# Kernel tuning notes

Measured on AMD Instinct MI355X. Metric: run time of the kernel, lower is better.

Reference implementation:

```python
import jax, jax.numpy as jnp
import numpy as np

B, T, F = 256, 2048, 20
H_NODES = 256


def _heaviside(x):
    # smooth heaviside approx used throughout the original module
    return (jnp.tanh(10.0 * x) + 1.0) * 0.5


def _evap(wu, wl, wd, pet):
    h = _heaviside
    et1 = h(wu - pet) * pet + h(pet - wu) * wu
    rp = h(pet - et1) * (pet - et1)  # h(-(pet-et1))*0 term vanishes
    et22 = h(rp - wl) * wl + h(wl - rp) * rp
    et2 = h(rp) * et22
    et33 = h(rp - et2 - wd) * wd + h(wd - (rp - et2)) * (rp - et2)
    et3 = h(rp - et2) * et33
    return et1, et2, et3


def _runoff(wu, wl, wd, p, wum, wlm, wdm, b, c):
    wum = wum * 19.9 + 0.1
    wlm = wlm * 30.0 + 60.0
    wdm = wdm * 60.0 + 60.0
    c = c * 0.19 + 0.01
    b = b * 0.3 + 0.1
    w_total = wum + wlm + wdm
    s = c * (wu / w_total) ** 2 + b * (wl / w_total) ** 2
    return _heaviside(p - s) * (p - s)


def _partition(runoff, k1, k2, k3):
    k1 = k1 * 0.69 + 0.01
    k2 = k2 * 0.69 + 0.01
    k3 = k3 * 0.89 + 0.01
    sr = k1 * runoff
    itf = k2 * (runoff - sr)
    bf = k3 * (runoff - sr - itf)
    return sr, itf, bf


def setup_inputs() -> dict:
    key = jax.random.key(0)
    ks = jax.random.split(key, 7)
    u = lambda k, shp: jax.random.uniform(k, shp, jnp.float32, -0.05, 0.05)
    inputs = jax.random.uniform(ks[0], (B, T, F), jnp.float32)
    return {
        "inputs": inputs,
        "w1": u(ks[1], (15, H_NODES)),
        "b1": jnp.zeros((H_NODES,), jnp.float32),
        "w2": u(ks[2], (H_NODES, 64)),
        "b2": jnp.zeros((64,), jnp.float32),
        "w3": u(ks[3], (64, 8)),
        "b3": jnp.zeros((8,), jnp.float32),
    }


def reference(inputs, w1, b1, w2, b2, w3, b3):
    pet = inputs[..., 0:1]
    tmean = inputs[..., 1:2]
    p = inputs[..., 2:3]
    attrs = inputs[..., 5:]  # [B,T,15]

    # static-attribute -> physical-parameter MLP
    h1 = jnp.tanh(attrs @ w1 + b1)
    h2 = jnp.tanh(h1 @ w2 + b2)
    params = jax.nn.sigmoid(h2 @ w3 + b3)  # [B,T,8]

    xs = jnp.concatenate([pet, p, tmean, params], axis=-1)  # [B,T,11]

    def step(state, x):
        wu, wl, wd = state[:, 0:1], state[:, 1:2], state[:, 2:3]
        pet_t, p_t = x[:, 0:1], x[:, 1:2]
        et1, et2, et3 = _evap(wu, wl, wd, pet_t)
        clip = lambda d: jnp.clip(d, -1e5, 1e5)
        wu_n = wu + clip(p_t - et1)
        wl_n = wl + clip(p_t - et1 - et2)
        wd_n = wd + clip(p_t - et1 - et2 - et3)
        ns = jnp.concatenate([wu_n, wl_n, wd_n], axis=1)  # [B,3]
        return ns, ns

    init = jnp.zeros((inputs.shape[0], 3), inputs.dtype)
    _, outs = jax.lax.scan(step, init, jnp.swapaxes(xs, 0, 1))  # [T,B,3]
    outputs = jnp.swapaxes(outs, 0, 1)  # [B,T,3]

    wu, wl, wd = outputs[..., 0:1], outputs[..., 1:2], outputs[..., 2:3]
    wum, wlm, wdm = params[..., 0:1], params[..., 1:2], params[..., 2:3]
    b, c = params[..., 3:4], params[..., 4:5]
    k1, k2, k3 = params[..., 5:6], params[..., 6:7], params[..., 7:8]

    et1, et2, et3 = _evap(wu, wl, wd, pet)
    # NOTE: original call() swaps (wl,wd) and (wlm,wdm) here - kept faithful
    runoff = _runoff(wu, wd, wl, p, wum, wdm, wlm, b, c)
    sr, itf, bf = _partition(runoff, k1, k2, k3)
    total_q = sr + itf * 0.5 + bf * 0.25  # flow routing
    return total_q  # [B,T,1]
```

## Files before the change

### kernel.cpp

```cpp
#include <hip/hip_runtime.h>

#define B_ 256
#define T_ 2048
#define F_ 20
#define NT (B_*T_)
#define CH 16
#define NCH (T_/CH)

typedef __bf16 bf16x8 __attribute__((ext_vector_type(8)));
typedef float  f32x4  __attribute__((ext_vector_type(4)));

__device__ __forceinline__ float ex2(float x){ return __builtin_amdgcn_exp2f(x); }
__device__ __forceinline__ float rcpf_(float x){ return __builtin_amdgcn_rcpf(x); }

#define K10F 28.853900817779268f
#define K1F   2.8853900817779268f
#define LOG2E 1.4426950408889634f

__device__ __forceinline__ float hside(float x){ return 1.0f - rcpf_(ex2(K10F*x) + 1.0f); }
__device__ __forceinline__ float tanh_f(float z){ return 1.0f - 2.0f*rcpf_(ex2(K1F*z) + 1.0f); }
__device__ __forceinline__ float sigmoid_f(float z){ return rcpf_(1.0f + ex2(-LOG2E*z)); }


__global__ __launch_bounds__(256) void prep_kernel(const float* __restrict__ in,
                                                   float* __restrict__ ws){
  int r = blockIdx.x*256 + threadIdx.x;
  if (r >= NT) return;
  int b = r & (B_-1);
  int t = r >> 8;
  const float* src = in + ((size_t)b*T_ + t)*F_;
  ((float2*)ws)[r] = make_float2(src[0], src[2]);
}

__global__ __launch_bounds__(512) void fused_kernel(const float* __restrict__ in,
    const float* __restrict__ w1, const float* __restrict__ b1,
    const float* __restrict__ w2, const float* __restrict__ b2,
    const float* __restrict__ w3, const float* __restrict__ b3,
    float* __restrict__ ws){
  extern __shared__ char sm[];
  float* pk4 = ws + 4*(size_t)NT;

  if (blockIdx.x < 4) {
    asm volatile("s_setprio 3");
    const float2* pp2 = (const float2*)ws;
    float* wuT = ws + 2*(size_t)NT;
    float* wdT = ws + 3*(size_t)NT;
    float*  d1L = (float*)sm;
    float*  bsQ = (float*)(sm + 8192);
    float2* rhL = (float2*)(sm + 24576);
    float2* qbL = (float2*)(sm + 40960);

    int tid = threadIdx.x;
    int wv = tid >> 6, lane = tid & 63;
    int boff = blockIdx.x * 64;

    float wu = 0.0f, wl = 0.0f, wd = 0.0f;
    float2 buf[2][8];

    if (wv == 0){
      #pragma unroll
      for (int g = 0; g < 2; ++g)
        #pragma unroll
        for (int i = 0; i < 8; ++i)
          buf[g][i] = pp2[(g*8 + i)*B_ + boff + lane];
    }

    for (int it = 0; it < NCH + 3; ++it){
      if (wv == 0){
        if (it < NCH){
          int c = it, par = c & 1;
          #pragma unroll
          for (int g = 0; g < 2; ++g){
            #pragma unroll
            for (int i = 0; i < 8; ++i){
              int s = g*8 + i;
              float pet = buf[g][i].x, p = buf[g][i].y;
              float d  = wu - pet;
              float r1 = rcpf_(ex2(K10F*d) + 1.0f);
              float d1 = -d*r1;
              float base = (p - pet) + d1;
              wu += base;
              wuT[(c*CH + s)*B_ + boff + lane] = wu;
              d1L[par*(CH*64) + s*64 + lane] = d1;
              bsQ[(c&3)*(CH*64) + s*64 + lane] = base;
            }
            int cn = (c + 1 < NCH) ? c + 1 : c;
            #pragma unroll
            for (int i = 0; i < 8; ++i)
              buf[g][i] = pp2[(cn*CH + g*8 + i)*B_ + boff + lane];
          }
        }
      } else if (wv == 1){
        if (it >= 1 && it <= NCH){
          int c = it - 1, par = c & 1;
          #pragma unroll
          for (int s = 0; s < CH; ++s){
            float d1 = d1L[par*(CH*64) + s*64 + lane];
            float r2 = rcpf_(ex2(K10F*d1) + 1.0f);
            float rp = fmaf(-d1, r2, d1);
            float hrp = 1.0f - rcpf_(ex2(K10F*rp) + 1.0f);
            rhL[par*(CH*64) + s*64 + lane] = make_float2(rp, hrp);
          }
        }
      } else if (wv == 2){
        if (it >= 2 && it <= NCH + 1){
          int c = it - 2, par = c & 1;
          #pragma unroll
          for (int s = 0; s < CH; ++s){
            float2 rh  = rhL[par*(CH*64) + s*64 + lane];
            float base = bsQ[(c&3)*(CH*64) + s*64 + lane];
            float d2   = rh.x - wl;
            float r    = rcpf_(ex2(K10F*d2) + 1.0f);
            float et22 = fmaf(d2, r, wl);
            float et2  = rh.y * et22;
            float b2   = base - et2;
            wl += b2;
            qbL[par*(CH*64) + s*64 + lane] = make_float2(rh.x - et2, b2);
          }
        }
      } else if (wv == 3){
        if (it >= 3){
          int c = it - 3, par = c & 1;
          #pragma unroll
          for (int s = 0; s < CH; ++s){
            float2 qb  = qbL[par*(CH*64) + s*64 + lane];
            float hqv  = 1.0f - rcpf_(ex2(K10F*qb.x) + 1.0f);
            float d3   = qb.x - wd;
            float r    = rcpf_(ex2(K10F*d3) + 1.0f);
            float et33 = fmaf(d3, r, wd);
            float et3  = hqv * et33;
            wd += qb.y - et3;
            wdT[(c*CH + s)*B_ + boff + lane] = wd;
          }
        }
      }
      __syncthreads();
    }
    return;
  }

  __bf16* w1f  = (__bf16*)sm;
  __bf16* w2f  = (__bf16*)(sm + 8192);
  float*  b1s  = (float*)(sm + 40960);
  float*  b2s  = (float*)(sm + 41984);
  float*  w3s  = (float*)(sm + 42240);
  float*  b3s  = (float*)(sm + 44288);
  __bf16* hbufA= (__bf16*)(sm + 44320);

  int tid = threadIdx.x;

  for (int s = tid; s < 16*32*8; s += 512) w1f[s] = (__bf16)0.0f;
  __syncthreads();
  for (int idx = tid; idx < 15*256; idx += 512){
    int k = idx >> 8, n = idx & 255;
    int ct = n >> 4;
    int l  = ((k>>3)*16) + (n & 15);
    int j  = k & 7;
    w1f[(ct*32 + l)*8 + j] = (__bf16)w1[idx];
  }
  for (int idx = tid; idx < 256*64; idx += 512){
    int k = idx >> 6, n = idx & 63;
    int kb = k >> 5;
    int lq = (k >> 3) & 3;
    int j  = k & 7;
    int ct = n >> 4;
    int l  = lq*16 + (n & 15);
    w2f[((kb*4 + ct)*64 + l)*8 + j] = (__bf16)w2[idx];
  }
  if (tid < 256) b1s[tid] = b1[tid];
  if (tid < 64)  b2s[tid] = b2[tid];
  if (tid < 512) w3s[tid] = w3[tid];
  if (tid < 8)   b3s[tid] = b3[tid];
  __syncthreads();

  int lane = tid & 63;
  int wv   = tid >> 6;
  int m    = lane & 15;
  int q    = lane >> 4;
  int r0   = (blockIdx.x - 4)*128 + wv*16;

  int rowA = r0 + m;
  int bA = rowA & (B_-1), tA = rowA >> 8;
  const float* ap = in + ((size_t)bA*T_ + tA)*F_ + 5;
  bf16x8 a1;
  #pragma unroll
  for (int j = 0; j < 8; ++j){
    int k = q*8 + j;
    float v = (k < 15) ? ap[k] : 0.0f;
    a1[j] = (__bf16)v;
  }

  __bf16* hb = hbufA + wv*1152;
  f32x4 zero4 = {0.0f, 0.0f, 0.0f, 0.0f};
  bf16x8 zero8;
  #pragma unroll
  for (int j = 0; j < 8; ++j) zero8[j] = (__bf16)0.0f;

  f32x4 acc2[4] = {zero4, zero4, zero4, zero4};

  #pragma unroll
  for (int p = 0; p < 4; ++p){
    #pragma unroll
    for (int c4 = 0; c4 < 4; ++c4){
      int ct = p*4 + c4;
      bf16x8 bw = zero8;
      if (lane < 32) bw = *(const bf16x8*)&w1f[(ct*32 + lane)*8];
      f32x4 c1 = __builtin_amdgcn_mfma_f32_16x16x32_bf16(a1, bw, zero4, 0, 0, 0);
      int f = c4*16 + m;
      float bb = b1s[p*64 + f];
      #pragma unroll
      for (int i = 0; i < 4; ++i){
        float h = tanh_f(c1[i] + bb);
        hb[(q*4 + i)*72 + f] = (__bf16)h;
      }
    }
    #pragma unroll
    for (int kb = 0; kb < 2; ++kb){
      bf16x8 a2 = *(const bf16x8*)&hb[m*72 + q*8 + kb*32];
      #pragma unroll
      for (int ct = 0; ct < 4; ++ct){
        bf16x8 bw2 = *(const bf16x8*)&w2f[(((p*2 + kb)*4 + ct)*64 + lane)*8];
        acc2[ct] = __builtin_amdgcn_mfma_f32_16x16x32_bf16(a2, bw2, acc2[ct], 0, 0, 0);
      }
    }
  }

  #pragma unroll
  for (int ct = 0; ct < 4; ++ct){
    int f = ct*16 + m;
    float bb = b2s[f];
    #pragma unroll
    for (int i = 0; i < 4; ++i){
      float h = tanh_f(acc2[ct][i] + bb);
      hb[(q*4 + i)*72 + f] = (__bf16)h;
    }
  }

  float z0 = b3s[2*q], z1 = b3s[2*q + 1];
  #pragma unroll
  for (int kb3 = 0; kb3 < 8; ++kb3){
    bf16x8 hv8 = *(const bf16x8*)&hb[m*72 + kb3*8];
    #pragma unroll
    for (int j = 0; j < 8; ++j){
      float hv = (float)hv8[j];
      int k = kb3*8 + j;
      z0 = fmaf(hv, w3s[k*8 + 2*q],     z0);
      z1 = fmaf(hv, w3s[k*8 + 2*q + 1], z1);
    }
  }

  float* hf = (float*)hb;
  hf[m*8 + 2*q]     = sigmoid_f(z0);
  hf[m*8 + 2*q + 1] = sigmoid_f(z1);
  if (q == 0){
    float P0=hf[m*8+0], P1=hf[m*8+1], P2=hf[m*8+2], P3=hf[m*8+3];
    float P4=hf[m*8+4], P5=hf[m*8+5], P6=hf[m*8+6], P7=hf[m*8+7];
    float wum = fmaf(P0, 19.9f, 0.1f);
    float wlm = fmaf(P2, 30.0f, 60.0f);
    float wdm = fmaf(P1, 60.0f, 60.0f);
    float wt  = wum + wlm + wdm;
    float rw  = 1.0f / wt;
    float cc  = fmaf(P4, 0.19f, 0.01f);
    float bc  = fmaf(P3, 0.30f, 0.10f);
    float A   = cc*rw*rw;
    float Bc  = bc*rw*rw;
    float k1  = fmaf(P5, 0.69f, 0.01f);
    float k2  = fmaf(P6, 0.69f, 0.01f);
    float k3  = fmaf(P7, 0.89f, 0.01f);
    float KP  = k1 + 0.5f*k2*(1.0f-k1) + 0.25f*k3*(1.0f-k1)*(1.0f-k2);
    int rowO = r0 + m;
    *(float4*)&pk4[(size_t)rowO*4] = make_float4(A, Bc, KP, 0.0f);
  }
}

__global__ __launch_bounds__(256) void final_kernel(const float* __restrict__ ws,
                                                    float* __restrict__ out){
  __shared__ float tile[64*65];
  int tb = blockIdx.x & 31;
  int bb = blockIdx.x >> 5;
  int t0 = tb*64, b0 = bb*64;
  int tid = threadIdx.x;
  const float2* pp2 = (const float2*)ws;
  const float* wuT  = ws + 2*(size_t)NT;
  const float* wdT  = ws + 3*(size_t)NT;
  const float* pk4  = ws + 4*(size_t)NT;

  #pragma unroll
  for (int k = 0; k < 16; ++k){
    int idx = k*256 + tid;
    int tl = idx >> 6, bl = idx & 63;
    int r = (t0 + tl)*B_ + b0 + bl;
    float p  = pp2[r].y;
    float wu = wuT[r], wd = wdT[r];
    float4 k4 = *(const float4*)&pk4[(size_t)r*4];
    float ps = p - k4.x*wu*wu - k4.y*wd*wd;
    float runoff = hside(ps)*ps;
    tile[bl*65 + tl] = k4.z * runoff;
  }
  __syncthreads();
  #pragma unroll
  for (int k = 0; k < 16; ++k){
    int idx = k*256 + tid;
    int tl2 = idx & 63, bl2 = idx >> 6;
    out[(size_t)(b0 + bl2)*T_ + t0 + tl2] = tile[bl2*65 + tl2];
  }
}

extern "C" void kernel_launch(void* const* d_in, const int* in_sizes, int n_in,
                              void* d_out, int out_size, void* d_ws, size_t ws_size,
                              hipStream_t stream) {
  const float* in = (const float*)d_in[0];
  const float* w1 = (const float*)d_in[1];
  const float* b1 = (const float*)d_in[2];
  const float* w2 = (const float*)d_in[3];
  const float* b2 = (const float*)d_in[4];
  const float* w3 = (const float*)d_in[5];
  const float* b3 = (const float*)d_in[6];
  float* out = (float*)d_out;
  float* ws  = (float*)d_ws;

  prep_kernel <<<NT/256,     256, 0,     stream>>>(in, ws);
  fused_kernel<<<NT/128 + 4, 512, 62752, stream>>>(in, w1, b1, w2, b2, w3, b3, ws);
  final_kernel<<<128,        256, 0,     stream>>>(ws, out);
}
```

Measured before the change: 215.4 us.

## Double rows per MLP block, stage w2 in halves, run layer3 on MFMA

Each wave of the MLP blocks now handles 32 rows instead of 16, which halves the block count and amortises per-block weight staging over twice the work. w2 is loaded into shared memory in two halves with extra barriers, so the shared footprint stays small. Layer 3 moves from scalar FMAs to MFMA, using a hi/lo bf16 split of w3 to keep precision close to the fp32 version. The costs are more registers per thread and extra synchronisation, and this may interact with the co-scheduled scan blocks that share the same grid.

```diff
diff --git a/kernel.cpp b/kernel.cpp
--- a/kernel.cpp
+++ b/kernel.cpp
@@ -113,9 +113,9 @@
             float r    = rcpf_(ex2(K10F*d2) + 1.0f);
             float et22 = fmaf(d2, r, wl);
             float et2  = rh.y * et22;
-            float b2   = base - et2;
-            wl += b2;
-            qbL[par*(CH*64) + s*64 + lane] = make_float2(rh.x - et2, b2);
+            float b2v  = base - et2;
+            wl += b2v;
+            qbL[par*(CH*64) + s*64 + lane] = make_float2(rh.x - et2, b2v);
           }
         }
       } else if (wv == 3){
@@ -139,17 +139,45 @@
     return;
   }
 
-  __bf16* w1f  = (__bf16*)sm;
-  __bf16* w2f  = (__bf16*)(sm + 8192);
-  float*  b1s  = (float*)(sm + 40960);
-  float*  b2s  = (float*)(sm + 41984);
-  float*  w3s  = (float*)(sm + 42240);
-  float*  b3s  = (float*)(sm + 44288);
-  __bf16* hbufA= (__bf16*)(sm + 44320);
-
-  int tid = threadIdx.x;
-
-  for (int s = tid; s < 16*32*8; s += 512) w1f[s] = (__bf16)0.0f;
+  __bf16* w1f   = (__bf16*)sm;
+  __bf16* w2f   = (__bf16*)(sm + 8192);
+  float*  b1s   = (float*)(sm + 24576);
+  float*  b2s   = (float*)(sm + 25600);
+  float*  b3s   = (float*)(sm + 25856);
+  __bf16* hbufA = (__bf16*)(sm + 25888);
+
+  int tid  = threadIdx.x;
+  int lane = tid & 63;
+  int wv   = tid >> 6;
+  int m    = lane & 15;
+  int q    = lane >> 4;
+  int r0   = (blockIdx.x - 4)*256 + wv*32;
+
+  bf16x8 a1[2];
+  #pragma unroll
+  for (int u = 0; u < 2; ++u){
+    int rowA = r0 + u*16 + m;
+    int bA = rowA & (B_-1), tA = rowA >> 8;
+    const float* ap = in + ((size_t)bA*T_ + tA)*F_ + 5;
+    #pragma unroll
+    for (int j = 0; j < 8; ++j){
+      int k = q*8 + j;
+      a1[u][j] = (__bf16)((k < 15) ? ap[k] : 0.0f);
+    }
+  }
+  bf16x8 w3h[2], w3l[2];
+  #pragma unroll
+  for (int kb = 0; kb < 2; ++kb){
+    #pragma unroll
+    for (int j = 0; j < 8; ++j){
+      float v = (m < 8) ? w3[(kb*32 + q*8 + j)*8 + m] : 0.0f;
+      __bf16 hi = (__bf16)v;
+      w3h[kb][j] = hi;
+      w3l[kb][j] = (__bf16)(v - (float)hi);
+    }
+  }
+
+  ((float4*)sm)[tid] = make_float4(0.0f, 0.0f, 0.0f, 0.0f);
   __syncthreads();
   for (int idx = tid; idx < 15*256; idx += 512){
     int k = idx >> 8, n = idx & 255;
@@ -158,69 +186,74 @@
     int j  = k & 7;
     w1f[(ct*32 + l)*8 + j] = (__bf16)w1[idx];
   }
-  for (int idx = tid; idx < 256*64; idx += 512){
-    int k = idx >> 6, n = idx & 63;
-    int kb = k >> 5;
-    int lq = (k >> 3) & 3;
-    int j  = k & 7;
-    int ct = n >> 4;
-    int l  = lq*16 + (n & 15);
-    w2f[((kb*4 + ct)*64 + l)*8 + j] = (__bf16)w2[idx];
+  for (int idx = tid; idx < 8192; idx += 512){
+    int kk = idx >> 6, n = idx & 63;
+    int kb2 = kk >> 5;
+    int lq  = (kk >> 3) & 3;
+    int j   = kk & 7;
+    int ct  = n >> 4;
+    int l   = lq*16 + (n & 15);
+    w2f[((kb2*4 + ct)*64 + l)*8 + j] = (__bf16)w2[kk*64 + n];
   }
   if (tid < 256) b1s[tid] = b1[tid];
   if (tid < 64)  b2s[tid] = b2[tid];
-  if (tid < 512) w3s[tid] = w3[tid];
   if (tid < 8)   b3s[tid] = b3[tid];
   __syncthreads();
 
-  int lane = tid & 63;
-  int wv   = tid >> 6;
-  int m    = lane & 15;
-  int q    = lane >> 4;
-  int r0   = (blockIdx.x - 4)*128 + wv*16;
-
-  int rowA = r0 + m;
-  int bA = rowA & (B_-1), tA = rowA >> 8;
-  const float* ap = in + ((size_t)bA*T_ + tA)*F_ + 5;
-  bf16x8 a1;
-  #pragma unroll
-  for (int j = 0; j < 8; ++j){
-    int k = q*8 + j;
-    float v = (k < 15) ? ap[k] : 0.0f;
-    a1[j] = (__bf16)v;
-  }
-
-  __bf16* hb = hbufA + wv*1152;
   f32x4 zero4 = {0.0f, 0.0f, 0.0f, 0.0f};
   bf16x8 zero8;
   #pragma unroll
   for (int j = 0; j < 8; ++j) zero8[j] = (__bf16)0.0f;
 
-  f32x4 acc2[4] = {zero4, zero4, zero4, zero4};
-
-  #pragma unroll
-  for (int p = 0; p < 4; ++p){
-    #pragma unroll
-    for (int c4 = 0; c4 < 4; ++c4){
-      int ct = p*4 + c4;
-      bf16x8 bw = zero8;
-      if (lane < 32) bw = *(const bf16x8*)&w1f[(ct*32 + lane)*8];
-      f32x4 c1 = __builtin_amdgcn_mfma_f32_16x16x32_bf16(a1, bw, zero4, 0, 0, 0);
-      int f = c4*16 + m;
-      float bb = b1s[p*64 + f];
-      #pragma unroll
-      for (int i = 0; i < 4; ++i){
-        float h = tanh_f(c1[i] + bb);
-        hb[(q*4 + i)*72 + f] = (__bf16)h;
-      }
-    }
-    #pragma unroll
-    for (int kb = 0; kb < 2; ++kb){
-      bf16x8 a2 = *(const bf16x8*)&hb[m*72 + q*8 + kb*32];
-      #pragma unroll
-      for (int ct = 0; ct < 4; ++ct){
-        bf16x8 bw2 = *(const bf16x8*)&w2f[(((p*2 + kb)*4 + ct)*64 + lane)*8];
-        acc2[ct] = __builtin_amdgcn_mfma_f32_16x16x32_bf16(a2, bw2, acc2[ct], 0, 0, 0);
+  __bf16* hb = hbufA + wv*2304;
+  f32x4 acc2[2][4] = {{zero4, zero4, zero4, zero4},
+                      {zero4, zero4, zero4, zero4}};
+
+  #pragma unroll
+  for (int pc = 0; pc < 2; ++pc){
+    if (pc == 1){
+      __syncthreads();
+      for (int idx = tid; idx < 8192; idx += 512){
+        int kk = idx >> 6, n = idx & 63;
+        int kb2 = kk >> 5;
+        int lq  = (kk >> 3) & 3;
+        int j   = kk & 7;
+        int ct  = n >> 4;
+        int l   = lq*16 + (n & 15);
+        w2f[((kb2*4 + ct)*64 + l)*8 + j] = (__bf16)w2[(128 + kk)*64 + n];
+      }
+      __syncthreads();
+    }
+    #pragma unroll
+    for (int ph = 0; ph < 2; ++ph){
+      int p = pc*2 + ph;
+      #pragma unroll
+      for (int c4 = 0; c4 < 4; ++c4){
+        int ct = p*4 + c4;
+        bf16x8 bw = zero8;
+        if (lane < 32) bw = *(const bf16x8*)&w1f[(ct*32 + lane)*8];
+        int f = c4*16 + m;
+        float bb = b1s[p*64 + f];
+        #pragma unroll
+        for (int u = 0; u < 2; ++u){
+          f32x4 c1 = __builtin_amdgcn_mfma_f32_16x16x32_bf16(a1[u], bw, zero4, 0, 0, 0);
+          #pragma unroll
+          for (int i = 0; i < 4; ++i){
+            float h = tanh_f(c1[i] + bb);
+            hb[(u*16 + q*4 + i)*72 + f] = (__bf16)h;
+          }
+        }
+      }
+      #pragma unroll
+      for (int kb = 0; kb < 2; ++kb){
+        bf16x8 a2_0 = *(const bf16x8*)&hb[ m      *72 + kb*32 + q*8];
+        bf16x8 a2_1 = *(const bf16x8*)&hb[(16 + m)*72 + kb*32 + q*8];
+        #pragma unroll
+        for (int ct = 0; ct < 4; ++ct){
+          bf16x8 bw2 = *(const bf16x8*)&w2f[(((ph*2 + kb)*4 + ct)*64 + lane)*8];
+          acc2[0][ct] = __builtin_amdgcn_mfma_f32_16x16x32_bf16(a2_0, bw2, acc2[0][ct], 0, 0, 0);
+          acc2[1][ct] = __builtin_amdgcn_mfma_f32_16x16x32_bf16(a2_1, bw2, acc2[1][ct], 0, 0, 0);
+        }
       }
     }
   }
@@ -230,31 +263,38 @@
     int f = ct*16 + m;
     float bb = b2s[f];
     #pragma unroll
-    for (int i = 0; i < 4; ++i){
-      float h = tanh_f(acc2[ct][i] + bb);
-      hb[(q*4 + i)*72 + f] = (__bf16)h;
-    }
-  }
-
-  float z0 = b3s[2*q], z1 = b3s[2*q + 1];
-  #pragma unroll
-  for (int kb3 = 0; kb3 < 8; ++kb3){
-    bf16x8 hv8 = *(const bf16x8*)&hb[m*72 + kb3*8];
-    #pragma unroll
-    for (int j = 0; j < 8; ++j){
-      float hv = (float)hv8[j];
-      int k = kb3*8 + j;
-      z0 = fmaf(hv, w3s[k*8 + 2*q],     z0);
-      z1 = fmaf(hv, w3s[k*8 + 2*q + 1], z1);
-    }
+    for (int u = 0; u < 2; ++u)
+      #pragma unroll
+      for (int i = 0; i < 4; ++i){
+        float h = tanh_f(acc2[u][ct][i] + bb);
+        hb[(u*16 + q*4 + i)*72 + f] = (__bf16)h;
+      }
+  }
+
+  f32x4 acc3[2] = {zero4, zero4};
+  #pragma unroll
+  for (int kb = 0; kb < 2; ++kb){
+    bf16x8 a3_0 = *(const bf16x8*)&hb[ m      *72 + kb*32 + q*8];
+    bf16x8 a3_1 = *(const bf16x8*)&hb[(16 + m)*72 + kb*32 + q*8];
+    acc3[0] = __builtin_amdgcn_mfma_f32_16x16x32_bf16(a3_0, w3h[kb], acc3[0], 0, 0, 0);
+    acc3[0] = __builtin_amdgcn_mfma_f32_16x16x32_bf16(a3_0, w3l[kb], acc3[0], 0, 0, 0);
+    acc3[1] = __builtin_amdgcn_mfma_f32_16x16x32_bf16(a3_1, w3h[kb], acc3[1], 0, 0, 0);
+    acc3[1] = __builtin_amdgcn_mfma_f32_16x16x32_bf16(a3_1, w3l[kb], acc3[1], 0, 0, 0);
   }
 
   float* hf = (float*)hb;
-  hf[m*8 + 2*q]     = sigmoid_f(z0);
-  hf[m*8 + 2*q + 1] = sigmoid_f(z1);
-  if (q == 0){
-    float P0=hf[m*8+0], P1=hf[m*8+1], P2=hf[m*8+2], P3=hf[m*8+3];
-    float P4=hf[m*8+4], P5=hf[m*8+5], P6=hf[m*8+6], P7=hf[m*8+7];
+  if (m < 8){
+    float bb3 = b3s[m];
+    #pragma unroll
+    for (int u = 0; u < 2; ++u)
+      #pragma unroll
+      for (int i = 0; i < 4; ++i)
+        hf[(u*16 + q*4 + i)*9 + m] = sigmoid_f(acc3[u][i] + bb3);
+  }
+  if (lane < 32){
+    const float* Pr = hf + lane*9;
+    float P0=Pr[0], P1=Pr[1], P2=Pr[2], P3=Pr[3];
+    float P4=Pr[4], P5=Pr[5], P6=Pr[6], P7=Pr[7];
     float wum = fmaf(P0, 19.9f, 0.1f);
     float wlm = fmaf(P2, 30.0f, 60.0f);
     float wdm = fmaf(P1, 60.0f, 60.0f);
@@ -268,8 +308,7 @@
     float k2  = fmaf(P6, 0.69f, 0.01f);
     float k3  = fmaf(P7, 0.89f, 0.01f);
     float KP  = k1 + 0.5f*k2*(1.0f-k1) + 0.25f*k3*(1.0f-k1)*(1.0f-k2);
-    int rowO = r0 + m;
-    *(float4*)&pk4[(size_t)rowO*4] = make_float4(A, Bc, KP, 0.0f);
+    *(float4*)&pk4[(size_t)(r0 + lane)*4] = make_float4(A, Bc, KP, 0.0f);
   }
 }
 
@@ -320,6 +359,6 @@
   float* ws  = (float*)d_ws;
 
   prep_kernel <<<NT/256,     256, 0,     stream>>>(in, ws);
-  fused_kernel<<<NT/128 + 4, 512, 62752, stream>>>(in, w1, b1, w2, b2, w3, b3, ws);
+  fused_kernel<<<NT/256 + 4, 512, 62752, stream>>>(in, w1, b1, w2, b2, w3, b3, ws);
   final_kernel<<<128,        256, 0,     stream>>>(ws, out);
 }
```

Measured after the change: 215.6 us. Within noise of the previous version (+0.1%).
